# Performance work log

Hardware: AMD Instinct MI355X
Metric: run time of the kernel (lower is better)

## Reference

```python
import jax, jax.numpy as jnp
import numpy as np

# ROI Align config (module attributes in the original torch wrapper)
SPATIAL_SCALE = 0.25
POOLED_H = 7
POOLED_W = 7
SAMPLE_NUM = 2
ROI_END_MODE = 1  # Ascend: end coord gets +roi_end_mode before scaling


def setup_inputs() -> dict:
    key = jax.random.key(0)
    k_feat, k_b, k_xy, k_wh = jax.random.split(key, 4)
    B, C, H, W = 2, 256, 200, 200
    N = 1000
    feat = jax.random.normal(k_feat, (B, C, H, W), dtype=jnp.float32)
    img_h, img_w = H / SPATIAL_SCALE, W / SPATIAL_SCALE
    bidx = jax.random.randint(k_b, (N,), 0, B).astype(jnp.float32)
    xy = jax.random.uniform(k_xy, (N, 2), dtype=jnp.float32)
    wh = jax.random.uniform(k_wh, (N, 2), dtype=jnp.float32)
    x1 = xy[:, 0] * (img_w - 64.0)
    y1 = xy[:, 1] * (img_h - 64.0)
    x2 = x1 + 8.0 + wh[:, 0] * 200.0
    y2 = y1 + 8.0 + wh[:, 1] * 200.0
    rois = jnp.stack([bidx, x1, y1, x2, y2], axis=1)  # [N,5]
    return {"input": feat, "rois": rois}


def _axis_coords(start, bin_size, pooled, sn):
    # sample coord for grid index g: start + bin_size*(g+0.5)/sn, g in [0, pooled*sn)
    g = jnp.arange(pooled * sn, dtype=jnp.float32)
    return start[:, None] + bin_size[:, None] * (g[None, :] + 0.5) / sn  # [N, pooled*sn]


def _bilinear_1d(c, size):
    # returns (low_idx, high_idx, w_low, w_high, valid) for coordinate array c
    valid = (c >= -1.0) & (c <= size)
    cc = jnp.clip(c, 0.0, size - 1.0)
    lo = jnp.floor(cc).astype(jnp.int32)
    lo = jnp.clip(lo, 0, size - 1)
    hi = jnp.clip(lo + 1, 0, size - 1)
    frac = cc - lo.astype(jnp.float32)
    return lo, hi, 1.0 - frac, frac, valid


def roi_align(feat, rois):
    B, C, H, W = feat.shape
    N = rois.shape[0]
    bidx = rois[:, 0].astype(jnp.int32)
    off = float(ROI_END_MODE)
    x1 = rois[:, 1] * SPATIAL_SCALE
    y1 = rois[:, 2] * SPATIAL_SCALE
    x2 = (rois[:, 3] + off) * SPATIAL_SCALE
    y2 = (rois[:, 4] + off) * SPATIAL_SCALE
    roi_w = jnp.maximum(x2 - x1, 1.0)
    roi_h = jnp.maximum(y2 - y1, 1.0)
    bin_h = roi_h / POOLED_H
    bin_w = roi_w / POOLED_W

    ys = _axis_coords(y1, bin_h, POOLED_H, SAMPLE_NUM)  # [N, GY]
    xs = _axis_coords(x1, bin_w, POOLED_W, SAMPLE_NUM)  # [N, GX]
    yl, yh, wyl, wyh, vy = _bilinear_1d(ys, H)
    xl, xh, wxl, wxh, vx = _bilinear_1d(xs, W)

    b = bidx[:, None, None]

    def gather(yi, xi):
        # advanced indexing -> [N, GY, GX, C]
        return feat[b, :, yi[:, :, None], xi[:, None, :]]

    val = (wyl[:, :, None, None] * wxl[:, None, :, None] * gather(yl, xl)
           + wyl[:, :, None, None] * wxh[:, None, :, None] * gather(yl, xh)
           + wyh[:, :, None, None] * wxl[:, None, :, None] * gather(yh, xl)
           + wyh[:, :, None, None] * wxh[:, None, :, None] * gather(yh, xh))
    mask = (vy[:, :, None] & vx[:, None, :]).astype(val.dtype)[..., None]
    val = val * mask  # [N, GY, GX, C]

    # average pool over the SAMPLE_NUM x SAMPLE_NUM grid inside each bin
    val = val.reshape(N, POOLED_H, SAMPLE_NUM, POOLED_W, SAMPLE_NUM, C)
    out = val.mean(axis=(2, 4))  # [N, PH, PW, C]
    return jnp.transpose(out, (0, 3, 1, 2))  # [N, C, PH, PW]


def reference(input, rois):
    return roi_align(input, rois)
```

## Files before the change

### kernel.cpp

```cpp
#include <hip/hip_runtime.h>
#include <hip/hip_bf16.h>


constexpr int C_TOT  = 256;
constexpr int H_FEAT = 200;
constexpr int W_FEAT = 200;
constexpr int HW     = H_FEAT * W_FEAT;
constexpr int S_TOT  = 49;

__global__ __launch_bounds__(256) void nchw_to_nhwc_bf16_kernel(
    const float* __restrict__ feat,
    unsigned short* __restrict__ featT)
{
    __shared__ float tile[32][33];
    int tx = threadIdx.x;
    int ty = threadIdx.y;
    int s0 = blockIdx.x * 32;
    int c0 = blockIdx.y * 32;
    int b  = blockIdx.z;

    const float* src = feat + ((size_t)b * C_TOT) * HW;
    #pragma unroll
    for (int i = 0; i < 4; ++i) {
        int r = ty + i * 8;
        tile[r][tx] = src[(size_t)(c0 + r) * HW + (s0 + tx)];
    }
    __syncthreads();
    unsigned short* dst = featT + ((size_t)b * HW) * C_TOT;
    #pragma unroll
    for (int i = 0; i < 4; ++i) {
        int r = ty + i * 8;
        float x = tile[tx][r];
        unsigned int u = __float_as_uint(x);
        unsigned int rb = (u + 0x7fffu + ((u >> 16) & 1u)) >> 16;
        dst[(size_t)(s0 + r) * C_TOT + (c0 + tx)] = (unsigned short)rb;
    }
}

__global__ __launch_bounds__(512) void roi_align_nhwc_kernel(
    const unsigned short* __restrict__ featT,
    const float* __restrict__ rois,
    float* __restrict__ out,
    int N)
{
    __shared__ alignas(16) float tile[C_TOT * S_TOT];

    int n    = blockIdx.x;
    int tid  = threadIdx.x;
    int wave = tid >> 6;
    int lane = tid & 63;

    const float* r = rois + (size_t)n * 5;
    int   b  = (int)r[0];
    float x1 = r[1] * 0.25f;
    float y1 = r[2] * 0.25f;
    float x2 = (r[3] + 1.0f) * 0.25f;
    float y2 = (r[4] + 1.0f) * 0.25f;
    float bin_w = fmaxf(x2 - x1, 1.0f) * (1.0f / 7.0f);
    float bin_h = fmaxf(y2 - y1, 1.0f) * (1.0f / 7.0f);

    const unsigned short* fbase =
        featT + (size_t)b * HW * C_TOT + (size_t)lane * 4;

    for (int s = wave; s < S_TOT; s += 8) {
        int ph = s / 7;
        int pw = s - ph * 7;

        int   yoff[2][2];
        int   xoff[2][2];
        float wy[2][2], wx[2][2];
        #pragma unroll
        for (int i = 0; i < 2; ++i) {
            float gy  = (float)(2 * ph + i);
            float cy  = y1 + bin_h * ((gy + 0.5f) * 0.5f);
            bool  vy  = (cy >= -1.0f) && (cy <= (float)H_FEAT);
            float ccy = fminf(fmaxf(cy, 0.0f), (float)(H_FEAT - 1));
            int   ylo = (int)ccy;
            int   yhi = min(ylo + 1, H_FEAT - 1);
            float fy  = ccy - (float)ylo;
            yoff[i][0] = ylo * W_FEAT;
            yoff[i][1] = yhi * W_FEAT;
            wy[i][0] = vy ? (1.0f - fy) : 0.0f;
            wy[i][1] = vy ? fy          : 0.0f;

            float gx  = (float)(2 * pw + i);
            float cx  = x1 + bin_w * ((gx + 0.5f) * 0.5f);
            bool  vx  = (cx >= -1.0f) && (cx <= (float)W_FEAT);
            float ccx = fminf(fmaxf(cx, 0.0f), (float)(W_FEAT - 1));
            int   xlo = (int)ccx;
            int   xhi = min(xlo + 1, W_FEAT - 1);
            float fx  = ccx - (float)xlo;
            xoff[i][0] = xlo;
            xoff[i][1] = xhi;
            wx[i][0] = vx ? (1.0f - fx) : 0.0f;
            wx[i][1] = vx ? fx          : 0.0f;
        }

        float4 acc = make_float4(0.f, 0.f, 0.f, 0.f);
        #pragma unroll
        for (int iy = 0; iy < 2; ++iy)
        #pragma unroll
        for (int jy = 0; jy < 2; ++jy)
        #pragma unroll
        for (int ix = 0; ix < 2; ++ix)
        #pragma unroll
        for (int jx = 0; jx < 2; ++jx) {
            float w = wy[iy][jy] * wx[ix][jx];
            const ushort4 v = *reinterpret_cast<const ushort4*>(
                fbase + (size_t)(yoff[iy][jy] + xoff[ix][jx]) * C_TOT);
            float f0 = __uint_as_float((unsigned int)v.x << 16);
            float f1 = __uint_as_float((unsigned int)v.y << 16);
            float f2 = __uint_as_float((unsigned int)v.z << 16);
            float f3 = __uint_as_float((unsigned int)v.w << 16);
            acc.x = fmaf(w, f0, acc.x);
            acc.y = fmaf(w, f1, acc.y);
            acc.z = fmaf(w, f2, acc.z);
            acc.w = fmaf(w, f3, acc.w);
        }
        acc.x *= 0.25f; acc.y *= 0.25f; acc.z *= 0.25f; acc.w *= 0.25f;

        int c = lane * 4;
        tile[(c + 0) * S_TOT + s] = acc.x;
        tile[(c + 1) * S_TOT + s] = acc.y;
        tile[(c + 2) * S_TOT + s] = acc.z;
        tile[(c + 3) * S_TOT + s] = acc.w;
    }
    __syncthreads();

    const float4* t4 = reinterpret_cast<const float4*>(tile);
    float4* o4 = reinterpret_cast<float4*>(out + (size_t)n * (C_TOT * S_TOT));
    constexpr int Q = C_TOT * S_TOT / 4;
    for (int q = tid; q < Q; q += 512)
        o4[q] = t4[q];
}

constexpr int CPT = 4;
constexpr int CG  = C_TOT / CPT;

__global__ __launch_bounds__(256) void roi_align_direct_kernel(
    const float* __restrict__ feat,
    const float* __restrict__ rois,
    float* __restrict__ out,
    int N)
{
    int t = blockIdx.x * 256 + threadIdx.x;
    int total = N * CG * S_TOT;
    if (t >= total) return;

    int s   = t % S_TOT;
    int rem = t / S_TOT;
    int c0  = rem % CG;
    int n   = rem / CG;
    int ph  = s / 7;
    int pw  = s - ph * 7;

    const float* r = rois + (size_t)n * 5;
    int   b  = (int)r[0];
    float x1 = r[1] * 0.25f;
    float y1 = r[2] * 0.25f;
    float x2 = (r[3] + 1.0f) * 0.25f;
    float y2 = (r[4] + 1.0f) * 0.25f;
    float bin_w = fmaxf(x2 - x1, 1.0f) * (1.0f / 7.0f);
    float bin_h = fmaxf(y2 - y1, 1.0f) * (1.0f / 7.0f);

    int   roff[2][2], coff[2][2];
    float wy[2][2], wx[2][2];
    #pragma unroll
    for (int i = 0; i < 2; ++i) {
        float gy  = (float)(2 * ph + i);
        float cy  = y1 + bin_h * ((gy + 0.5f) * 0.5f);
        bool  vy  = (cy >= -1.0f) && (cy <= (float)H_FEAT);
        float ccy = fminf(fmaxf(cy, 0.0f), (float)(H_FEAT - 1));
        int   ylo = (int)ccy;
        int   yhi = min(ylo + 1, H_FEAT - 1);
        float fy  = ccy - (float)ylo;
        roff[i][0] = ylo * W_FEAT;
        roff[i][1] = yhi * W_FEAT;
        wy[i][0] = vy ? (1.0f - fy) : 0.0f;
        wy[i][1] = vy ? fy          : 0.0f;

        float gx  = (float)(2 * pw + i);
        float cx  = x1 + bin_w * ((gx + 0.5f) * 0.5f);
        bool  vx  = (cx >= -1.0f) && (cx <= (float)W_FEAT);
        float ccx = fminf(fmaxf(cx, 0.0f), (float)(W_FEAT - 1));
        int   xlo = (int)ccx;
        int   xhi = min(xlo + 1, W_FEAT - 1);
        float fx  = ccx - (float)xlo;
        coff[i][0] = xlo;
        coff[i][1] = xhi;
        wx[i][0] = vx ? (1.0f - fx) : 0.0f;
        wx[i][1] = vx ? fx          : 0.0f;
    }

    float w16[16];
    int   o16[16];
    #pragma unroll
    for (int iy = 0; iy < 2; ++iy)
    #pragma unroll
    for (int ix = 0; ix < 2; ++ix)
    #pragma unroll
    for (int jy = 0; jy < 2; ++jy)
    #pragma unroll
    for (int jx = 0; jx < 2; ++jx) {
        int idx = ((iy * 2 + ix) * 2 + jy) * 2 + jx;
        w16[idx] = wy[iy][jy] * wx[ix][jx];
        o16[idx] = roff[iy][jy] + coff[ix][jx];
    }

    size_t base  = ((size_t)b * C_TOT + c0) * HW;
    size_t obase = (size_t)n * (C_TOT * S_TOT) + (size_t)c0 * S_TOT + s;

    #pragma unroll
    for (int k = 0; k < CPT; ++k) {
        const float* f = feat + base + (size_t)k * CG * HW;
        float acc = 0.0f;
        #pragma unroll
        for (int j = 0; j < 16; ++j)
            acc = fmaf(w16[j], f[o16[j]], acc);
        out[obase + (size_t)k * (CG * S_TOT)] = acc * 0.25f;
    }
}

extern "C" void kernel_launch(void* const* d_in, const int* in_sizes, int n_in,
                              void* d_out, int out_size, void* d_ws, size_t ws_size,
                              hipStream_t stream) {
    const float* feat = (const float*)d_in[0];
    const float* rois = (const float*)d_in[1];
    float* out = (float*)d_out;
    int N = in_sizes[1] / 5;

    size_t nhwc_bytes = (size_t)2 * HW * C_TOT * sizeof(unsigned short);
    if (ws_size >= nhwc_bytes) {
        unsigned short* featT = (unsigned short*)d_ws;
        dim3 tgrid(HW / 32, C_TOT / 32, 2);
        dim3 tblk(32, 8);
        nchw_to_nhwc_bf16_kernel<<<tgrid, tblk, 0, stream>>>(feat, featT);
        roi_align_nhwc_kernel<<<N, 512, 0, stream>>>(featT, rois, out, N);
    } else {
        int total  = N * CG * S_TOT;
        int blocks = (total + 255) / 256;
        roi_align_direct_kernel<<<blocks, 256, 0, stream>>>(feat, rois, out, N);
    }
}
```

Before: 63.04 us.

## Sort ROIs by Morton order and map sorted chunks to XCDs for L2 locality

Adds a single-block bitonic sort kernel that orders ROIs by batch index and the Morton code of their center. The align kernel then remaps block IDs so that each XCD processes a contiguous chunk of spatially sorted ROIs, aiming to improve L2 reuse of the transposed feature map. It also folds the 0.25 averaging factor into the bilinear weights, removing a final multiply. The cost is an extra serial sort launch with many syncthreads, plus an extra indirection load per block.

```diff
diff --git a/kernel.cpp b/kernel.cpp
--- a/kernel.cpp
+++ b/kernel.cpp
@@ -7,6 +7,53 @@
 constexpr int W_FEAT = 200;
 constexpr int HW     = H_FEAT * W_FEAT;
 constexpr int S_TOT  = 49;
+constexpr size_t FEATT_BYTES = (size_t)2 * HW * C_TOT * sizeof(unsigned short);
+constexpr int NXCD = 8;
+
+__global__ __launch_bounds__(1024) void roi_sort_kernel(
+    const float* __restrict__ rois, int* __restrict__ perm, int N)
+{
+    __shared__ unsigned int skey[1024];
+    __shared__ unsigned short sval[1024];
+    int t = threadIdx.x;
+
+    unsigned int key = 0xFFFFFFFFu;
+    if (t < N) {
+        const float* r = rois + (size_t)t * 5;
+        int   b  = (int)r[0];
+        float cx = (r[1] + r[3]) * 0.5f * 0.25f;
+        float cy = (r[2] + r[4]) * 0.5f * 0.25f;
+        unsigned int ix = (unsigned int)min(max((int)cx, 0), W_FEAT - 1);
+        unsigned int iy = (unsigned int)min(max((int)cy, 0), H_FEAT - 1);
+        unsigned int m = 0;
+        #pragma unroll
+        for (int i = 0; i < 8; ++i) {
+            m |= ((ix >> i) & 1u) << (2 * i);
+            m |= ((iy >> i) & 1u) << (2 * i + 1);
+        }
+        key = ((unsigned int)b << 16) | m;
+    }
+    skey[t] = key;
+    sval[t] = (unsigned short)t;
+    __syncthreads();
+
+    for (int k = 2; k <= 1024; k <<= 1) {
+        for (int j = k >> 1; j > 0; j >>= 1) {
+            int p = t ^ j;
+            if (p > t) {
+                bool up = ((t & k) == 0);
+                unsigned int a = skey[t], c = skey[p];
+                if ((a > c) == up) {
+                    skey[t] = c; skey[p] = a;
+                    unsigned short va = sval[t], vc = sval[p];
+                    sval[t] = vc; sval[p] = va;
+                }
+            }
+            __syncthreads();
+        }
+    }
+    if (t < N) perm[t] = (int)sval[t];
+}
 
 __global__ __launch_bounds__(256) void nchw_to_nhwc_bf16_kernel(
     const float* __restrict__ feat,
@@ -40,12 +87,22 @@
 __global__ __launch_bounds__(512) void roi_align_nhwc_kernel(
     const unsigned short* __restrict__ featT,
     const float* __restrict__ rois,
+    const int* __restrict__ perm,
     float* __restrict__ out,
-    int N)
+    int N, int use_perm)
 {
     __shared__ alignas(16) float tile[C_TOT * S_TOT];
 
-    int n    = blockIdx.x;
+    int n;
+    if (use_perm) {
+        int chunk = (N + NXCD - 1) / NXCD;
+        int rank  = (blockIdx.x & (NXCD - 1)) * chunk + (blockIdx.x >> 3);
+        if (rank >= N) rank = blockIdx.x;
+        n = perm[rank];
+    } else {
+        n = blockIdx.x;
+    }
+
     int tid  = threadIdx.x;
     int wave = tid >> 6;
     int lane = tid & 63;
@@ -80,8 +137,8 @@
             float fy  = ccy - (float)ylo;
             yoff[i][0] = ylo * W_FEAT;
             yoff[i][1] = yhi * W_FEAT;
-            wy[i][0] = vy ? (1.0f - fy) : 0.0f;
-            wy[i][1] = vy ? fy          : 0.0f;
+            wy[i][0] = vy ? (1.0f - fy) * 0.5f : 0.0f;
+            wy[i][1] = vy ? fy * 0.5f          : 0.0f;
 
             float gx  = (float)(2 * pw + i);
             float cx  = x1 + bin_w * ((gx + 0.5f) * 0.5f);
@@ -92,8 +149,8 @@
             float fx  = ccx - (float)xlo;
             xoff[i][0] = xlo;
             xoff[i][1] = xhi;
-            wx[i][0] = vx ? (1.0f - fx) : 0.0f;
-            wx[i][1] = vx ? fx          : 0.0f;
+            wx[i][0] = vx ? (1.0f - fx) * 0.5f : 0.0f;
+            wx[i][1] = vx ? fx * 0.5f          : 0.0f;
         }
 
         float4 acc = make_float4(0.f, 0.f, 0.f, 0.f);
@@ -117,7 +174,6 @@
             acc.z = fmaf(w, f2, acc.z);
             acc.w = fmaf(w, f3, acc.w);
         }
-        acc.x *= 0.25f; acc.y *= 0.25f; acc.z *= 0.25f; acc.w *= 0.25f;
 
         int c = lane * 4;
         tile[(c + 0) * S_TOT + s] = acc.x;
@@ -229,13 +285,17 @@
     float* out = (float*)d_out;
     int N = in_sizes[1] / 5;
 
-    size_t nhwc_bytes = (size_t)2 * HW * C_TOT * sizeof(unsigned short);
-    if (ws_size >= nhwc_bytes) {
+    size_t need = FEATT_BYTES + 4096;
+    if (ws_size >= need) {
         unsigned short* featT = (unsigned short*)d_ws;
+        int* perm = (int*)((char*)d_ws + FEATT_BYTES);
+        int use_perm = (N <= 1024) ? 1 : 0;
+        if (use_perm)
+            roi_sort_kernel<<<1, 1024, 0, stream>>>(rois, perm, N);
         dim3 tgrid(HW / 32, C_TOT / 32, 2);
         dim3 tblk(32, 8);
         nchw_to_nhwc_bf16_kernel<<<tgrid, tblk, 0, stream>>>(feat, featT);
-        roi_align_nhwc_kernel<<<N, 512, 0, stream>>>(featT, rois, out, N);
+        roi_align_nhwc_kernel<<<N, 512, 0, stream>>>(featT, rois, perm, out, N, use_perm);
     } else {
         int total  = N * CG * S_TOT;
         int blocks = (total + 255) / 256;
```

After: 70.29 us. +11.5%, slower.
